# Performance work log

Hardware: AMD Instinct MI355X
Metric: run time of the kernel (lower is better)

## Reference

```python
import jax, jax.numpy as jnp
import numpy as np

N = 100000          # nodes
E = 1600000         # edges (avg degree 16)
D_IN = 128          # in_features
D_OUT = 128         # out_features


def setup_inputs() -> dict:
    key = jax.random.key(0)
    k1, k2, k3, k4 = jax.random.split(key, 4)
    H = jax.random.normal(k1, (N, D_IN), dtype=jnp.float32)
    # COO indices of sparse adjacency A: row i aggregates features of col j
    src = jax.random.randint(k2, (E,), 0, N, dtype=jnp.int32)
    dst = jax.random.randint(k3, (E,), 0, N, dtype=jnp.int32)
    # nn.Linear(2*in_features, out_features): weight [out, 2*in], zero bias
    W = jax.random.normal(k4, (D_OUT, 2 * D_IN), dtype=jnp.float32) * 0.05
    b = jnp.zeros((D_OUT,), dtype=jnp.float32)
    return {"H": H, "src": src, "dst": dst, "W": W, "b": b}


def reference(H, src, dst, W, b):
    # max-aggregation: for each node i, max over features of its neighbors.
    # One fused gather + segment-max replaces the per-node Python loop.
    gathered = H[dst]  # [E, D_IN]
    agg = jax.ops.segment_max(gathered, src, num_segments=N)  # [N, D_IN]
    # nodes with no incoming edges stay zero (torch code leaves zeros)
    deg = jax.ops.segment_sum(jnp.ones((src.shape[0],), jnp.float32), src,
                              num_segments=N)  # [N]
    H_neigh = jnp.where(deg[:, None] > 0, agg, 0.0)
    H_concat = jnp.concatenate([H, H_neigh], axis=1)  # [N, 2*D_IN]
    return H_concat @ W.T + b
```

## Files before the change

### kernel.cpp

```cpp
#include <hip/hip_runtime.h>
#include <math.h>

#define NN 100000
#define NE 1600000
#define DD 128
#define NB 3125
#define CAP 704

#define WS_HB  0
#define WS_CUR 6400000
#define WS_ENT 6403128
#define WS_AB  8603128
#define WS_END_AB (WS_AB + 6400000)

typedef __attribute__((ext_vector_type(8))) __bf16 bf8_t;
typedef __attribute__((ext_vector_type(4))) float f4_t;

__device__ __forceinline__ unsigned f2bf(float f) {
    unsigned u = __float_as_uint(f);
    u += 0x7FFFu + ((u >> 16) & 1u);
    return u >> 16;
}

__global__ __launch_bounds__(256) void conv_bf16_kernel(const float* __restrict__ src,
                                                        uint4* __restrict__ dst,
                                                        int n8) {
    int i = blockIdx.x * 256 + threadIdx.x;
    if (i >= n8) return;
    const float4* s = (const float4*)src + (size_t)i * 2;
    float4 a = s[0], b = s[1];
    uint4 o;
    o.x = f2bf(a.x) | (f2bf(a.y) << 16);
    o.y = f2bf(a.z) | (f2bf(a.w) << 16);
    o.z = f2bf(b.x) | (f2bf(b.y) << 16);
    o.w = f2bf(b.z) | (f2bf(b.w) << 16);
    dst[i] = o;
}

__global__ __launch_bounds__(256) void cursor_init_kernel(int* __restrict__ cursor) {
    int i = blockIdx.x * 256 + threadIdx.x;
    if (i < NB) cursor[i] = i * CAP;
}

__global__ __launch_bounds__(256) void partition_kernel(const int* __restrict__ src,
                                                        const int* __restrict__ dst,
                                                        int* __restrict__ bin_cursor,
                                                        unsigned* __restrict__ entries) {
    __shared__ int cnt[NB];
    __shared__ int gcur[NB];
    const int t = threadIdx.x;
    for (int i = t; i < NB; i += 256) cnt[i] = 0;
    __syncthreads();
    const int base = blockIdx.x * 8192;
    int sv[32];
#pragma unroll
    for (int k = 0; k < 32; ++k) {
        int e = base + k * 256 + t;
        sv[k] = (e < NE) ? src[e] : -1;
        if (e < NE) atomicAdd(&cnt[sv[k] >> 5], 1);
    }
    __syncthreads();
    for (int i = t; i < NB; i += 256) {
        int c = cnt[i];
        gcur[i] = c ? atomicAdd(&bin_cursor[i], c) : 0;
    }
    __syncthreads();
#pragma unroll
    for (int k = 0; k < 32; ++k) {
        int e = base + k * 256 + t;
        if (e < NE) {
            int s = sv[k];
            int pos = atomicAdd(&gcur[s >> 5], 1);
            entries[pos] = ((unsigned)(s & 31) << 17) | (unsigned)dst[e];
        }
    }
}

template <bool BF16OUT>
__global__ __launch_bounds__(256) void agg_sort_kernel(const unsigned short* __restrict__ Hb,
                                                       const int* __restrict__ bin_cursor,
                                                       const unsigned* __restrict__ entries,
                                                       unsigned* __restrict__ Ab,
                                                       float* __restrict__ aggf) {
    __shared__ unsigned raw[CAP];
    __shared__ unsigned sorted[CAP];
    __shared__ int cnt[32], base_s[32], cur[32];
    const int t = threadIdx.x;
    const int b = blockIdx.x;
    const int beg = b * CAP;
    const int n = bin_cursor[b] - beg;

    if (t < 32) cnt[t] = 0;
    __syncthreads();
    for (int i = t; i < n; i += 256) {
        unsigned e = entries[beg + i];
        raw[i] = e;
        atomicAdd(&cnt[e >> 17], 1);
    }
    __syncthreads();
    if (t < 32) {
        int v = cnt[t];
        int incl = v;
#pragma unroll
        for (int o = 1; o < 32; o <<= 1) {
            int y = __shfl_up(incl, o, 64);
            if (t >= o) incl += y;
        }
        base_s[t] = incl - v;
        cur[t] = incl - v;
    }
    __syncthreads();
    for (int i = t; i < n; i += 256) {
        unsigned e = raw[i];
        int pos = atomicAdd(&cur[e >> 17], 1);
        sorted[pos] = e & 0x1FFFFu;
    }
    __syncthreads();

    const int lane = t & 63;
    const int w = t >> 6;
#pragma unroll
    for (int q = 0; q < 8; ++q) {
        int ln = w * 8 + q;
        int s0 = base_s[ln];
        int e0 = s0 + cnt[ln];
        float mx = 0.f, my = 0.f;
        if (s0 < e0) {
            mx = -INFINITY; my = -INFINITY;
            int j = s0;
            for (; j + 4 <= e0; j += 4) {
                unsigned d0 = sorted[j], d1 = sorted[j + 1];
                unsigned d2 = sorted[j + 2], d3 = sorted[j + 3];
                unsigned v0 = *(const unsigned*)(Hb + (size_t)d0 * DD + lane * 2);
                unsigned v1 = *(const unsigned*)(Hb + (size_t)d1 * DD + lane * 2);
                unsigned v2 = *(const unsigned*)(Hb + (size_t)d2 * DD + lane * 2);
                unsigned v3 = *(const unsigned*)(Hb + (size_t)d3 * DD + lane * 2);
                float x0 = __uint_as_float(v0 << 16), y0 = __uint_as_float(v0 & 0xFFFF0000u);
                float x1 = __uint_as_float(v1 << 16), y1 = __uint_as_float(v1 & 0xFFFF0000u);
                float x2 = __uint_as_float(v2 << 16), y2 = __uint_as_float(v2 & 0xFFFF0000u);
                float x3 = __uint_as_float(v3 << 16), y3 = __uint_as_float(v3 & 0xFFFF0000u);
                mx = fmaxf(mx, fmaxf(fmaxf(x0, x1), fmaxf(x2, x3)));
                my = fmaxf(my, fmaxf(fmaxf(y0, y1), fmaxf(y2, y3)));
            }
            for (; j < e0; ++j) {
                unsigned d0 = sorted[j];
                unsigned v0 = *(const unsigned*)(Hb + (size_t)d0 * DD + lane * 2);
                mx = fmaxf(mx, __uint_as_float(v0 << 16));
                my = fmaxf(my, __uint_as_float(v0 & 0xFFFF0000u));
            }
        }
        int node = b * 32 + ln;
        if (BF16OUT) {
            unsigned pv = (__float_as_uint(mx) >> 16) | (__float_as_uint(my) & 0xFFFF0000u);
            Ab[(size_t)node * 64 + lane] = pv;
        } else {
            *(float2*)(aggf + (size_t)node * DD + lane * 2) = make_float2(mx, my);
        }
    }
}

#define XP 72
template <bool BF16AGG>
__global__ __launch_bounds__(256) void mfma_matmul_kernel(
        const unsigned short* __restrict__ Hb,
        const unsigned short* __restrict__ Ab,
        const float* __restrict__ W,
        const float* __restrict__ bias,
        float* __restrict__ out) {
    __shared__ unsigned short Xs[64 * XP];
    __shared__ unsigned short Ws[128 * XP];
    const int t = threadIdx.x;
    const int lane = t & 63;
    const int w = t >> 6;
    const int quad = lane >> 4;
    const int l16 = lane & 15;
    const int blockrow = blockIdx.x * 64;

    f4_t acc[8] = {};

    for (int c = 0; c < 4; ++c) {
        const int k0 = c * 64;
        if (BF16AGG || c < 2) {
            const unsigned short* xb = (c < 2) ? Hb : Ab;
            const int koff = (c < 2) ? k0 : k0 - 128;
            int seg = t & 7, r0 = t >> 3;
#pragma unroll
            for (int j = 0; j < 2; ++j) {
                int r = r0 + 32 * j;
                int row = blockrow + r;
                uint4 v = make_uint4(0, 0, 0, 0);
                if (row < NN)
                    v = *(const uint4*)(xb + (size_t)row * DD + koff + seg * 8);
                *(uint4*)&Xs[r * XP + seg * 8] = v;
            }
        } else {
            int seg = t & 15, r0 = t >> 4;
#pragma unroll
            for (int j = 0; j < 4; ++j) {
                int r = r0 + 16 * j;
                int row = blockrow + r;
                float4 v = make_float4(0.f, 0.f, 0.f, 0.f);
                if (row < NN)
                    v = *(const float4*)(out + (size_t)row * DD + (k0 - 128) + seg * 4);
                uint2 p;
                p.x = f2bf(v.x) | (f2bf(v.y) << 16);
                p.y = f2bf(v.z) | (f2bf(v.w) << 16);
                *(uint2*)&Xs[r * XP + seg * 4] = p;
            }
        }
        {
            int seg = t & 15, o0 = t >> 4;
#pragma unroll
            for (int j = 0; j < 8; ++j) {
                int o = o0 + 16 * j;
                float4 wv = *(const float4*)(W + (size_t)o * 256 + k0 + seg * 4);
                uint2 p;
                p.x = f2bf(wv.x) | (f2bf(wv.y) << 16);
                p.y = f2bf(wv.z) | (f2bf(wv.w) << 16);
                *(uint2*)&Ws[o * XP + seg * 4] = p;
            }
        }
        __syncthreads();
#pragma unroll
        for (int kk = 0; kk < 64; kk += 32) {
            bf8_t a = *(const bf8_t*)&Xs[(w * 16 + l16) * XP + kk + quad * 8];
#pragma unroll
            for (int ot = 0; ot < 8; ++ot) {
                bf8_t bf = *(const bf8_t*)&Ws[(ot * 16 + l16) * XP + kk + quad * 8];
                acc[ot] = __builtin_amdgcn_mfma_f32_16x16x32_bf16(a, bf, acc[ot], 0, 0, 0);
            }
        }
        __syncthreads();
    }

#pragma unroll
    for (int ot = 0; ot < 8; ++ot) {
        float bv = bias[ot * 16 + l16];
#pragma unroll
        for (int reg = 0; reg < 4; ++reg) {
            int row = blockrow + w * 16 + quad * 4 + reg;
            if (row < NN)
                out[(size_t)row * DD + ot * 16 + l16] = acc[ot][reg] + bv;
        }
    }
}

extern "C" void kernel_launch(void* const* d_in, const int* in_sizes, int n_in,
                              void* d_out, int out_size, void* d_ws, size_t ws_size,
                              hipStream_t stream) {
    const float* H   = (const float*)d_in[0];
    const int*   src = (const int*)d_in[1];
    const int*   dst = (const int*)d_in[2];
    const float* W   = (const float*)d_in[3];
    const float* b   = (const float*)d_in[4];
    float* out = (float*)d_out;

    int* ws = (int*)d_ws;
    unsigned short* Hb      = (unsigned short*)(ws + WS_HB);
    int*            cursor  = ws + WS_CUR;
    unsigned*       entries = (unsigned*)(ws + WS_ENT);
    unsigned*       Ab      = (unsigned*)(ws + WS_AB);

    const bool use_ab = ws_size >= (size_t)WS_END_AB * 4;

    const int h8 = NN * DD / 8;
    conv_bf16_kernel<<<(h8 + 255) / 256, 256, 0, stream>>>(H, (uint4*)Hb, h8);
    cursor_init_kernel<<<(NB + 255) / 256, 256, 0, stream>>>(cursor);
    partition_kernel<<<(NE + 8191) / 8192, 256, 0, stream>>>(src, dst, cursor, entries);

    if (use_ab) {
        agg_sort_kernel<true><<<NB, 256, 0, stream>>>(Hb, cursor, entries, Ab, out);
        mfma_matmul_kernel<true><<<(NN + 63) / 64, 256, 0, stream>>>(
            Hb, (const unsigned short*)Ab, W, b, out);
    } else {
        agg_sort_kernel<false><<<NB, 256, 0, stream>>>(Hb, cursor, entries, Ab, out);
        mfma_matmul_kernel<false><<<(NN + 63) / 64, 256, 0, stream>>>(
            Hb, (const unsigned short*)Ab, W, b, out);
    }
}
```

Before: 269.4 us.

## Switch to fp16 packed max, fuse conversion with partition, widen bins to 64 nodes

Moves the feature copy from bf16 to fp16 so aggregation can use packed half2 max on the raw 32-bit words instead of unpacking to float, and switches the matmul to f16 MFMA. Folds the H conversion and the edge partition into one launch with two block roles, and doubles the bin width to 64 nodes per aggregation block with larger capacity. The fallback path that wrote fp32 aggregates into the output when the workspace was small is removed. This trades bf16 range for fp16 precision (values outside fp16 range would saturate) and assumes the workspace is always large enough.

```diff
diff --git a/kernel.cpp b/kernel.cpp
--- a/kernel.cpp
+++ b/kernel.cpp
@@ -4,105 +4,112 @@
 #define NN 100000
 #define NE 1600000
 #define DD 128
-#define NB 3125
-#define CAP 704
-
-#define WS_HB  0
+#define NB 1563
+#define CAP 1280
+#define PB 196
+#define CB 196
+
+#define WS_HH  0
 #define WS_CUR 6400000
-#define WS_ENT 6403128
-#define WS_AB  8603128
-#define WS_END_AB (WS_AB + 6400000)
-
-typedef __attribute__((ext_vector_type(8))) __bf16 bf8_t;
+#define WS_ENT (WS_CUR + NB)
+#define WS_AH  (WS_ENT + NB * CAP)
+
+typedef __attribute__((ext_vector_type(8))) _Float16 h8_t;
+typedef __attribute__((ext_vector_type(2))) _Float16 h2_t;
 typedef __attribute__((ext_vector_type(4))) float f4_t;
 
-__device__ __forceinline__ unsigned f2bf(float f) {
-    unsigned u = __float_as_uint(f);
-    u += 0x7FFFu + ((u >> 16) & 1u);
-    return u >> 16;
-}
-
-__global__ __launch_bounds__(256) void conv_bf16_kernel(const float* __restrict__ src,
-                                                        uint4* __restrict__ dst,
-                                                        int n8) {
-    int i = blockIdx.x * 256 + threadIdx.x;
-    if (i >= n8) return;
-    const float4* s = (const float4*)src + (size_t)i * 2;
-    float4 a = s[0], b = s[1];
-    uint4 o;
-    o.x = f2bf(a.x) | (f2bf(a.y) << 16);
-    o.y = f2bf(a.z) | (f2bf(a.w) << 16);
-    o.z = f2bf(b.x) | (f2bf(b.y) << 16);
-    o.w = f2bf(b.z) | (f2bf(b.w) << 16);
-    dst[i] = o;
-}
-
-__global__ __launch_bounds__(256) void cursor_init_kernel(int* __restrict__ cursor) {
-    int i = blockIdx.x * 256 + threadIdx.x;
+__device__ __forceinline__ unsigned pk2h(float x, float y) {
+    h2_t h;
+    h.x = (_Float16)x;
+    h.y = (_Float16)y;
+    return *(unsigned*)&h;
+}
+
+__device__ __forceinline__ h2_t h2max(h2_t a, h2_t b) {
+    return __builtin_elementwise_max(a, b);
+}
+
+__global__ __launch_bounds__(1024) void cursor_init_kernel(int* __restrict__ cursor) {
+    int i = blockIdx.x * 1024 + threadIdx.x;
     if (i < NB) cursor[i] = i * CAP;
 }
 
-__global__ __launch_bounds__(256) void partition_kernel(const int* __restrict__ src,
-                                                        const int* __restrict__ dst,
-                                                        int* __restrict__ bin_cursor,
-                                                        unsigned* __restrict__ entries) {
+__global__ __launch_bounds__(1024) void prep_kernel(const float* __restrict__ H,
+                                                    const int* __restrict__ src,
+                                                    const int* __restrict__ dst,
+                                                    int* __restrict__ cursor,
+                                                    unsigned* __restrict__ entries,
+                                                    uint4* __restrict__ Hh4) {
     __shared__ int cnt[NB];
     __shared__ int gcur[NB];
     const int t = threadIdx.x;
-    for (int i = t; i < NB; i += 256) cnt[i] = 0;
-    __syncthreads();
-    const int base = blockIdx.x * 8192;
-    int sv[32];
-#pragma unroll
-    for (int k = 0; k < 32; ++k) {
-        int e = base + k * 256 + t;
-        sv[k] = (e < NE) ? src[e] : -1;
-        if (e < NE) atomicAdd(&cnt[sv[k] >> 5], 1);
-    }
-    __syncthreads();
-    for (int i = t; i < NB; i += 256) {
-        int c = cnt[i];
-        gcur[i] = c ? atomicAdd(&bin_cursor[i], c) : 0;
-    }
-    __syncthreads();
-#pragma unroll
-    for (int k = 0; k < 32; ++k) {
-        int e = base + k * 256 + t;
-        if (e < NE) {
-            int s = sv[k];
-            int pos = atomicAdd(&gcur[s >> 5], 1);
-            entries[pos] = ((unsigned)(s & 31) << 17) | (unsigned)dst[e];
-        }
-    }
-}
-
-template <bool BF16OUT>
-__global__ __launch_bounds__(256) void agg_sort_kernel(const unsigned short* __restrict__ Hb,
-                                                       const int* __restrict__ bin_cursor,
-                                                       const unsigned* __restrict__ entries,
-                                                       unsigned* __restrict__ Ab,
-                                                       float* __restrict__ aggf) {
+    const int b = blockIdx.x;
+    if (b < PB) {
+        for (int i = t; i < NB; i += 1024) cnt[i] = 0;
+        __syncthreads();
+        const int base = b * 8192;
+        int sv[8];
+#pragma unroll
+        for (int k = 0; k < 8; ++k) {
+            int e = base + k * 1024 + t;
+            sv[k] = (e < NE) ? src[e] : -1;
+            if (sv[k] >= 0) atomicAdd(&cnt[sv[k] >> 6], 1);
+        }
+        __syncthreads();
+        for (int i = t; i < NB; i += 1024) {
+            int c = cnt[i];
+            gcur[i] = c ? atomicAdd(&cursor[i], c) : 0;
+        }
+        __syncthreads();
+#pragma unroll
+        for (int k = 0; k < 8; ++k) {
+            int e = base + k * 1024 + t;
+            if (sv[k] >= 0) {
+                int s = sv[k];
+                int pos = atomicAdd(&gcur[s >> 6], 1);
+                entries[pos] = ((unsigned)(s & 63) << 17) | (unsigned)dst[e];
+            }
+        }
+    } else {
+        const int nb = b - PB;
+        const int n8 = NN * DD / 8;
+        for (int i = nb * 1024 + t; i < n8; i += CB * 1024) {
+            const float4* s = (const float4*)H + (size_t)i * 2;
+            float4 a = s[0], c4 = s[1];
+            uint4 o;
+            o.x = pk2h(a.x, a.y);
+            o.y = pk2h(a.z, a.w);
+            o.z = pk2h(c4.x, c4.y);
+            o.w = pk2h(c4.z, c4.w);
+            Hh4[i] = o;
+        }
+    }
+}
+
+__global__ __launch_bounds__(256) void agg_kernel(const _Float16* __restrict__ Hh,
+                                                  const int* __restrict__ cursor,
+                                                  const unsigned* __restrict__ entries,
+                                                  unsigned* __restrict__ Ah) {
     __shared__ unsigned raw[CAP];
     __shared__ unsigned sorted[CAP];
-    __shared__ int cnt[32], base_s[32], cur[32];
+    __shared__ int cnt[64], base_s[64], cur[64];
     const int t = threadIdx.x;
     const int b = blockIdx.x;
-    const int beg = b * CAP;
-    const int n = bin_cursor[b] - beg;
-
-    if (t < 32) cnt[t] = 0;
+    const int n = cursor[b] - b * CAP;
+
+    if (t < 64) cnt[t] = 0;
     __syncthreads();
     for (int i = t; i < n; i += 256) {
-        unsigned e = entries[beg + i];
+        unsigned e = entries[b * CAP + i];
         raw[i] = e;
         atomicAdd(&cnt[e >> 17], 1);
     }
     __syncthreads();
-    if (t < 32) {
+    if (t < 64) {
         int v = cnt[t];
         int incl = v;
 #pragma unroll
-        for (int o = 1; o < 32; o <<= 1) {
+        for (int o = 1; o < 64; o <<= 1) {
             int y = __shfl_up(incl, o, 64);
             if (t >= o) incl += y;
         }
@@ -120,50 +127,38 @@
     const int lane = t & 63;
     const int w = t >> 6;
 #pragma unroll
-    for (int q = 0; q < 8; ++q) {
-        int ln = w * 8 + q;
+    for (int q = 0; q < 16; ++q) {
+        int ln = w * 16 + q;
         int s0 = base_s[ln];
         int e0 = s0 + cnt[ln];
-        float mx = 0.f, my = 0.f;
-        if (s0 < e0) {
-            mx = -INFINITY; my = -INFINITY;
-            int j = s0;
-            for (; j + 4 <= e0; j += 4) {
-                unsigned d0 = sorted[j], d1 = sorted[j + 1];
-                unsigned d2 = sorted[j + 2], d3 = sorted[j + 3];
-                unsigned v0 = *(const unsigned*)(Hb + (size_t)d0 * DD + lane * 2);
-                unsigned v1 = *(const unsigned*)(Hb + (size_t)d1 * DD + lane * 2);
-                unsigned v2 = *(const unsigned*)(Hb + (size_t)d2 * DD + lane * 2);
-                unsigned v3 = *(const unsigned*)(Hb + (size_t)d3 * DD + lane * 2);
-                float x0 = __uint_as_float(v0 << 16), y0 = __uint_as_float(v0 & 0xFFFF0000u);
-                float x1 = __uint_as_float(v1 << 16), y1 = __uint_as_float(v1 & 0xFFFF0000u);
-                float x2 = __uint_as_float(v2 << 16), y2 = __uint_as_float(v2 & 0xFFFF0000u);
-                float x3 = __uint_as_float(v3 << 16), y3 = __uint_as_float(v3 & 0xFFFF0000u);
-                mx = fmaxf(mx, fmaxf(fmaxf(x0, x1), fmaxf(x2, x3)));
-                my = fmaxf(my, fmaxf(fmaxf(y0, y1), fmaxf(y2, y3)));
-            }
-            for (; j < e0; ++j) {
-                unsigned d0 = sorted[j];
-                unsigned v0 = *(const unsigned*)(Hb + (size_t)d0 * DD + lane * 2);
-                mx = fmaxf(mx, __uint_as_float(v0 << 16));
-                my = fmaxf(my, __uint_as_float(v0 & 0xFFFF0000u));
-            }
-        }
-        int node = b * 32 + ln;
-        if (BF16OUT) {
-            unsigned pv = (__float_as_uint(mx) >> 16) | (__float_as_uint(my) & 0xFFFF0000u);
-            Ab[(size_t)node * 64 + lane] = pv;
-        } else {
-            *(float2*)(aggf + (size_t)node * DD + lane * 2) = make_float2(mx, my);
+        unsigned mu = 0xFC00FC00u;
+        h2_t m = *(h2_t*)&mu;
+        int j = s0;
+        for (; j + 4 <= e0; j += 4) {
+            unsigned d0 = sorted[j], d1 = sorted[j + 1];
+            unsigned d2 = sorted[j + 2], d3 = sorted[j + 3];
+            h2_t v0 = *(const h2_t*)(Hh + (size_t)d0 * DD + lane * 2);
+            h2_t v1 = *(const h2_t*)(Hh + (size_t)d1 * DD + lane * 2);
+            h2_t v2 = *(const h2_t*)(Hh + (size_t)d2 * DD + lane * 2);
+            h2_t v3 = *(const h2_t*)(Hh + (size_t)d3 * DD + lane * 2);
+            m = h2max(m, h2max(h2max(v0, v1), h2max(v2, v3)));
+        }
+        for (; j < e0; ++j) {
+            h2_t v0 = *(const h2_t*)(Hh + (size_t)sorted[j] * DD + lane * 2);
+            m = h2max(m, v0);
+        }
+        int node = b * 64 + ln;
+        if (node < NN) {
+            unsigned outv = (s0 < e0) ? *(unsigned*)&m : 0u;
+            Ah[(size_t)node * 64 + lane] = outv;
         }
     }
 }
 
 #define XP 72
-template <bool BF16AGG>
 __global__ __launch_bounds__(256) void mfma_matmul_kernel(
-        const unsigned short* __restrict__ Hb,
-        const unsigned short* __restrict__ Ab,
+        const unsigned short* __restrict__ Hh,
+        const unsigned short* __restrict__ Ah,
         const float* __restrict__ W,
         const float* __restrict__ bias,
         float* __restrict__ out) {
@@ -180,8 +175,8 @@
 
     for (int c = 0; c < 4; ++c) {
         const int k0 = c * 64;
-        if (BF16AGG || c < 2) {
-            const unsigned short* xb = (c < 2) ? Hb : Ab;
+        {
+            const unsigned short* xb = (c < 2) ? Hh : Ah;
             const int koff = (c < 2) ? k0 : k0 - 128;
             int seg = t & 7, r0 = t >> 3;
 #pragma unroll
@@ -193,20 +188,6 @@
                     v = *(const uint4*)(xb + (size_t)row * DD + koff + seg * 8);
                 *(uint4*)&Xs[r * XP + seg * 8] = v;
             }
-        } else {
-            int seg = t & 15, r0 = t >> 4;
-#pragma unroll
-            for (int j = 0; j < 4; ++j) {
-                int r = r0 + 16 * j;
-                int row = blockrow + r;
-                float4 v = make_float4(0.f, 0.f, 0.f, 0.f);
-                if (row < NN)
-                    v = *(const float4*)(out + (size_t)row * DD + (k0 - 128) + seg * 4);
-                uint2 p;
-                p.x = f2bf(v.x) | (f2bf(v.y) << 16);
-                p.y = f2bf(v.z) | (f2bf(v.w) << 16);
-                *(uint2*)&Xs[r * XP + seg * 4] = p;
-            }
         }
         {
             int seg = t & 15, o0 = t >> 4;
@@ -215,19 +196,19 @@
                 int o = o0 + 16 * j;
                 float4 wv = *(const float4*)(W + (size_t)o * 256 + k0 + seg * 4);
                 uint2 p;
-                p.x = f2bf(wv.x) | (f2bf(wv.y) << 16);
-                p.y = f2bf(wv.z) | (f2bf(wv.w) << 16);
+                p.x = pk2h(wv.x, wv.y);
+                p.y = pk2h(wv.z, wv.w);
                 *(uint2*)&Ws[o * XP + seg * 4] = p;
             }
         }
         __syncthreads();
 #pragma unroll
         for (int kk = 0; kk < 64; kk += 32) {
-            bf8_t a = *(const bf8_t*)&Xs[(w * 16 + l16) * XP + kk + quad * 8];
+            h8_t a = *(const h8_t*)&Xs[(w * 16 + l16) * XP + kk + quad * 8];
 #pragma unroll
             for (int ot = 0; ot < 8; ++ot) {
-                bf8_t bf = *(const bf8_t*)&Ws[(ot * 16 + l16) * XP + kk + quad * 8];
-                acc[ot] = __builtin_amdgcn_mfma_f32_16x16x32_bf16(a, bf, acc[ot], 0, 0, 0);
+                h8_t bf = *(const h8_t*)&Ws[(ot * 16 + l16) * XP + kk + quad * 8];
+                acc[ot] = __builtin_amdgcn_mfma_f32_16x16x32_f16(a, bf, acc[ot], 0, 0, 0);
             }
         }
         __syncthreads();
@@ -256,25 +237,14 @@
     float* out = (float*)d_out;
 
     int* ws = (int*)d_ws;
-    unsigned short* Hb      = (unsigned short*)(ws + WS_HB);
+    unsigned short* Hh      = (unsigned short*)(ws + WS_HH);
     int*            cursor  = ws + WS_CUR;
     unsigned*       entries = (unsigned*)(ws + WS_ENT);
-    unsigned*       Ab      = (unsigned*)(ws + WS_AB);
-
-    const bool use_ab = ws_size >= (size_t)WS_END_AB * 4;
-
-    const int h8 = NN * DD / 8;
-    conv_bf16_kernel<<<(h8 + 255) / 256, 256, 0, stream>>>(H, (uint4*)Hb, h8);
-    cursor_init_kernel<<<(NB + 255) / 256, 256, 0, stream>>>(cursor);
-    partition_kernel<<<(NE + 8191) / 8192, 256, 0, stream>>>(src, dst, cursor, entries);
-
-    if (use_ab) {
-        agg_sort_kernel<true><<<NB, 256, 0, stream>>>(Hb, cursor, entries, Ab, out);
-        mfma_matmul_kernel<true><<<(NN + 63) / 64, 256, 0, stream>>>(
-            Hb, (const unsigned short*)Ab, W, b, out);
-    } else {
-        agg_sort_kernel<false><<<NB, 256, 0, stream>>>(Hb, cursor, entries, Ab, out);
-        mfma_matmul_kernel<false><<<(NN + 63) / 64, 256, 0, stream>>>(
-            Hb, (const unsigned short*)Ab, W, b, out);
-    }
-}
+    unsigned*       Ah      = (unsigned*)(ws + WS_AH);
+
+    cursor_init_kernel<<<2, 1024, 0, stream>>>(cursor);
+    prep_kernel<<<PB + CB, 1024, 0, stream>>>(H, src, dst, cursor, entries, (uint4*)Hh);
+    agg_kernel<<<NB, 256, 0, stream>>>((const _Float16*)Hh, cursor, entries, Ah);
+    mfma_matmul_kernel<<<(NN + 63) / 64, 256, 0, stream>>>(
+        Hh, (const unsigned short*)Ah, W, b, out);
+}
```

New measurement: 239.8 us. -11.0%, faster.
